# Kernel optimization log

Hardware: AMD Instinct MI355X
Metric: run time of the kernel (lower is better)

The kernel has to match this reference:

```python
import jax, jax.numpy as jnp
import numpy as np

LN_EPS = 1e-5

def _layer_norm(x, gamma, beta):
    m = jnp.mean(x, axis=-1, keepdims=True)
    v = jnp.mean((x - m) ** 2, axis=-1, keepdims=True)
    return (x - m) / jnp.sqrt(v + LN_EPS) * gamma + beta

def setup_inputs() -> dict:
    key = jax.random.key(0)
    k1, k2, k3 = jax.random.split(key, 3)
    N, E, D = 8192, 4096, 128
    node_embeddings = jax.random.normal(k1, (N, D), dtype=jnp.float32)
    target_matrix = jax.random.normal(k2, (N, N), dtype=jnp.float32)
    hypergraph_matrix = jax.random.randint(k3, (N, E), 0, 2, dtype=jnp.int32)
    ln_gamma = jnp.ones((D,), dtype=jnp.float32)
    ln_beta = jnp.zeros((D,), dtype=jnp.float32)
    return {
        "node_embeddings": node_embeddings,
        "target_matrix": target_matrix,
        "ln_gamma": ln_gamma,
        "ln_beta": ln_beta,
        "hypergraph_matrix": hypergraph_matrix,
        "num_layers": 3,
    }

def reference(node_embeddings, target_matrix, ln_gamma, ln_beta, hypergraph_matrix, num_layers):
    x = node_embeddings  # [N, D]
    for _ in range(num_layers):
        t = jnp.matmul(target_matrix, x)        # [N, D]
        x = jnp.matmul(target_matrix.T, t)      # [N, D]
        x = _layer_norm(x, ln_gamma, ln_beta)
        # dropout is identity in eval mode
    # per-hyperedge masked mean over nodes, vectorized as a dense GEMV-style reduce
    h = (hypergraph_matrix > 0).astype(x.dtype)            # [N, E]
    counts = jnp.sum(h, axis=0)                            # [E]
    sums = jnp.einsum('ne,nd->ed', h, x)                   # [E, D]
    means = sums / counts[:, None]                         # [E, D]
    return jnp.max(means, axis=0)                          # [D]
```

## Files before the change

### kernel.cpp

```cpp
#include <hip/hip_runtime.h>
#include <cstdint>
#include <cstddef>

typedef __attribute__((ext_vector_type(8))) short short8;
typedef __attribute__((ext_vector_type(4))) short short4v;
typedef __attribute__((ext_vector_type(4))) float float4v;
typedef __attribute__((ext_vector_type(4))) int int4v;
typedef unsigned short ushort_t;

__device__ __forceinline__ ushort_t f2bf(float f) {
  unsigned u = __builtin_bit_cast(unsigned, f);
  u = (u + 0x7FFFu + ((u >> 16) & 1u)) >> 16;
  return (ushort_t)u;
}
__device__ __forceinline__ float bf2f(ushort_t h) {
  unsigned u = ((unsigned)h) << 16;
  return __builtin_bit_cast(float, u);
}

__device__ __forceinline__ void gld_lds16(const void* g, void* l) {
  __builtin_amdgcn_global_load_lds(
      (const __attribute__((address_space(1))) void*)g,
      (__attribute__((address_space(3))) void*)l, 16, 0, 0);
}

__global__ __launch_bounds__(256, 3) void gemm_tn(
    const ushort_t* __restrict__ A, const ushort_t* __restrict__ B,
    float* __restrict__ P, int M, int N, int K) {
  __shared__ ushort_t As[128 * 64];
  __shared__ ushort_t Bs[128 * 64];
  const int tid = threadIdx.x;
  const int lane = tid & 63;
  const int wave = tid >> 6;
  const int wm = (wave & 1) * 64;
  const int wn = (wave >> 1) * 64;
  const int m0 = blockIdx.x * 128;
  const int n0 = blockIdx.y * 128;
  int t0, tl;
  if (blockIdx.z < 8) { t0 = blockIdx.z * 11; tl = 11; }
  else { t0 = 88 + (blockIdx.z - 8) * 10; tl = 10; }
  float* __restrict__ Pc = P + (size_t)blockIdx.z * M * N;

  float4v acc[4][4] = {};

  for (int t = t0; t < t0 + tl; t++) {
    const ushort_t* Ag = A + (size_t)m0 * K + t * 64;
    const ushort_t* Bg = B + (size_t)n0 * K + t * 64;
#pragma unroll
    for (int i = 0; i < 4; i++) {
      int f = i * 4096 + tid * 16;
      int r = f >> 7;
      int cb = f & 127;
      gld_lds16((const char*)(Ag + (size_t)r * K) + cb, (char*)As + f);
      gld_lds16((const char*)(Bg + (size_t)r * K) + cb, (char*)Bs + f);
    }
    __syncthreads();
#pragma unroll
    for (int ks = 0; ks < 64; ks += 32) {
      short8 af[4], bfr[4];
      const int kr = ks + (lane >> 4) * 8;
      const int l15 = lane & 15;
#pragma unroll
      for (int im = 0; im < 4; im++)
        af[im] = *(const short8*)&As[(wm + im * 16 + l15) * 64 + kr];
#pragma unroll
      for (int in = 0; in < 4; in++)
        bfr[in] = *(const short8*)&Bs[(wn + in * 16 + l15) * 64 + kr];
#pragma unroll
      for (int im = 0; im < 4; im++)
#pragma unroll
        for (int in = 0; in < 4; in++)
          acc[im][in] = __builtin_amdgcn_mfma_f32_16x16x32_bf16(
              af[im], bfr[in], acc[im][in], 0, 0, 0);
    }
    __syncthreads();
  }
  const int cn = lane & 15;
  const int cr = (lane >> 4) * 4;
#pragma unroll
  for (int im = 0; im < 4; im++)
#pragma unroll
    for (int in = 0; in < 4; in++)
#pragma unroll
      for (int r = 0; r < 4; r++) {
        int m = wm + im * 16 + cr + r;
        int n = wn + in * 16 + cn;
        Pc[(size_t)(m0 + m) * N + (n0 + n)] = acc[im][in][r];
      }
}

__global__ __launch_bounds__(256, 3) void gemm_nn(
    const ushort_t* __restrict__ A, const ushort_t* __restrict__ B,
    float* __restrict__ P, int M, int N, int K) {
  __shared__ ushort_t As[128 * 64];
  __shared__ ushort_t Bs[64 * 128];
  const int tid = threadIdx.x;
  const int lane = tid & 63;
  const int wave = tid >> 6;
  const int wm = (wave & 1) * 64;
  const int wn = (wave >> 1) * 64;
  const int m0 = blockIdx.x * 128;
  const int n0 = blockIdx.y * 128;
  int t0, tl;
  if (blockIdx.z < 8) { t0 = blockIdx.z * 11; tl = 11; }
  else { t0 = 88 + (blockIdx.z - 8) * 10; tl = 10; }
  float* __restrict__ Pc = P + (size_t)blockIdx.z * M * N;

  int brow[4], bcol[4];
#pragma unroll
  for (int i = 0; i < 4; i++) {
    const int c = i * 256 + tid;
    brow[i] = ((c >> 6) << 2) | ((c >> 1) & 3);
    bcol[i] = (((c >> 3) & 7) << 4) | ((c & 1) << 3);
  }
  const int l15 = lane & 15;
  const int hi = lane >> 4;
  const unsigned BsB =
      (unsigned)(uintptr_t)(__attribute__((address_space(3))) void*)Bs;
  const unsigned trb = BsB + (unsigned)(hi * 2048) + (unsigned)(l15 * 8);

  float4v acc[4][4] = {};

  for (int t = t0; t < t0 + tl; t++) {
    const ushort_t* Ag = A + (size_t)m0 * K + t * 64;
    const ushort_t* Bg = B + (size_t)(t * 64) * N + n0;
#pragma unroll
    for (int i = 0; i < 4; i++) {
      int f = i * 4096 + tid * 16;
      int r = f >> 7;
      int cb = f & 127;
      gld_lds16((const char*)(Ag + (size_t)r * K) + cb, (char*)As + f);
      gld_lds16((const char*)(Bg + (size_t)brow[i] * N + bcol[i]),
                (char*)Bs + f);
    }
    __syncthreads();
#pragma unroll
    for (int ks = 0; ks < 64; ks += 32) {
      short8 af[4];
      const int kr = ks + hi * 8;
#pragma unroll
      for (int im = 0; im < 4; im++)
        af[im] = *(const short8*)&As[(wm + im * 16 + l15) * 64 + kr];
      short4v r0[4], r1[4];
      const unsigned tb = trb + (unsigned)((ks >> 2) * 1024) + (unsigned)(wn * 8);
#pragma unroll
      for (int in = 0; in < 4; in++) {
        asm volatile(
            "ds_read_b64_tr_b16 %0, %2\n\t"
            "ds_read_b64_tr_b16 %1, %2 offset:1024"
            : "=&v"(r0[in]), "=&v"(r1[in])
            : "v"(tb + (unsigned)(in * 128)));
      }
      asm volatile("s_waitcnt lgkmcnt(0)" ::: "memory");
      __builtin_amdgcn_sched_barrier(0);
#pragma unroll
      for (int im = 0; im < 4; im++)
#pragma unroll
        for (int in = 0; in < 4; in++) {
          short8 bf8 = __builtin_shufflevector(r0[in], r1[in],
                                               0, 1, 2, 3, 4, 5, 6, 7);
          acc[im][in] = __builtin_amdgcn_mfma_f32_16x16x32_bf16(
              af[im], bf8, acc[im][in], 0, 0, 0);
        }
    }
    __syncthreads();
  }
  const int cn = lane & 15;
  const int cr = (lane >> 4) * 4;
#pragma unroll
  for (int im = 0; im < 4; im++)
#pragma unroll
    for (int in = 0; in < 4; in++)
#pragma unroll
      for (int r = 0; r < 4; r++) {
        int m = wm + im * 16 + cr + r;
        int n = wn + in * 16 + cn;
        Pc[(size_t)(m0 + m) * N + (n0 + n)] = acc[im][in][r];
      }
}

__global__ __launch_bounds__(256) void cast32_k(
    const float* __restrict__ src, ushort_t* __restrict__ dst) {
  const size_t i = ((size_t)blockIdx.x * 256 + threadIdx.x) * 8;
  float4v a = *(const float4v*)(src + i);
  float4v b = *(const float4v*)(src + i + 4);
  ushort_t o[8];
  o[0] = f2bf(a.x); o[1] = f2bf(a.y); o[2] = f2bf(a.z); o[3] = f2bf(a.w);
  o[4] = f2bf(b.x); o[5] = f2bf(b.y); o[6] = f2bf(b.z); o[7] = f2bf(b.w);
  *(short8*)&dst[i] = *(const short8*)o;
}

__global__ __launch_bounds__(256) void dualcast_f32_k(
    const float* __restrict__ src, ushort_t* __restrict__ dstN,
    ushort_t* __restrict__ dstT, int R, int C) {
  __shared__ float tile[64][65];
  const int c0 = blockIdx.x * 64, r0 = blockIdx.y * 64;
  const int tr = threadIdx.x >> 2, cs = (threadIdx.x & 3) * 16;
  const float* s = src + (size_t)(r0 + tr) * C + c0 + cs;
  float v[16];
#pragma unroll
  for (int j = 0; j < 16; j += 4) {
    float4v t4 = *(const float4v*)(s + j);
    v[j] = t4.x; v[j + 1] = t4.y; v[j + 2] = t4.z; v[j + 3] = t4.w;
  }
  if (dstN) {
    ushort_t o[16];
#pragma unroll
    for (int j = 0; j < 16; j++) o[j] = f2bf(v[j]);
    ushort_t* d = dstN + (size_t)(r0 + tr) * C + c0 + cs;
    *(short8*)d = *(const short8*)&o[0];
    *(short8*)(d + 8) = *(const short8*)&o[8];
  }
#pragma unroll
  for (int j = 0; j < 16; j++) tile[tr][cs + j] = v[j];
  __syncthreads();
  const int tc = threadIdx.x >> 2, rs = (threadIdx.x & 3) * 16;
  ushort_t o[16];
#pragma unroll
  for (int j = 0; j < 16; j++) o[j] = f2bf(tile[rs + j][tc]);
  ushort_t* d = dstT + (size_t)(c0 + tc) * R + r0 + rs;
  *(short8*)d = *(const short8*)&o[0];
  *(short8*)(d + 8) = *(const short8*)&o[8];
}

__global__ __launch_bounds__(256) void tcast_i32_k(
    const int* __restrict__ src, ushort_t* __restrict__ dstT,
    float* __restrict__ partial, int R, int C) {
  __shared__ float tile[64][65];
  const int c0 = blockIdx.x * 64, r0 = blockIdx.y * 64;
  const int tr = threadIdx.x >> 2, cs = (threadIdx.x & 3) * 16;
  const int* s = src + (size_t)(r0 + tr) * C + c0 + cs;
#pragma unroll
  for (int j = 0; j < 16; j += 4) {
    int4v t4 = *(const int4v*)(s + j);
    tile[tr][cs + j] = t4.x > 0 ? 1.f : 0.f;
    tile[tr][cs + j + 1] = t4.y > 0 ? 1.f : 0.f;
    tile[tr][cs + j + 2] = t4.z > 0 ? 1.f : 0.f;
    tile[tr][cs + j + 3] = t4.w > 0 ? 1.f : 0.f;
  }
  __syncthreads();
  const int tc = threadIdx.x >> 2, rs = (threadIdx.x & 3) * 16;
  ushort_t o[16];
#pragma unroll
  for (int j = 0; j < 16; j++) o[j] = f2bf(tile[rs + j][tc]);
  ushort_t* d = dstT + (size_t)(c0 + tc) * R + r0 + rs;
  *(short8*)d = *(const short8*)&o[0];
  *(short8*)(d + 8) = *(const short8*)&o[8];
  if (threadIdx.x < 64) {
    float sum = 0.f;
#pragma unroll
    for (int r = 0; r < 64; r++) sum += tile[r][threadIdx.x];
    partial[(size_t)(r0 >> 6) * C + c0 + threadIdx.x] = sum;
  }
}

__global__ __launch_bounds__(256) void counts2_k(
    const float* __restrict__ partial, float* __restrict__ counts, int E) {
  const int e = blockIdx.x * 256 + threadIdx.x;
  float s = 0.f;
  for (int r = 0; r < 128; r++) s += partial[(size_t)r * E + e];
  counts[e] = s;
}

__global__ __launch_bounds__(256) void cast_k(
    const float* __restrict__ P, ushort_t* __restrict__ out, int MN) {
  const int i = (blockIdx.x * 256 + threadIdx.x) * 8;
  float4v a = {0.f, 0.f, 0.f, 0.f}, b = {0.f, 0.f, 0.f, 0.f};
  for (int sp = 0; sp < 12; sp++) {
    a += *(const float4v*)&P[(size_t)sp * MN + i];
    b += *(const float4v*)&P[(size_t)sp * MN + i + 4];
  }
  ushort_t o[8];
  o[0] = f2bf(a.x); o[1] = f2bf(a.y); o[2] = f2bf(a.z); o[3] = f2bf(a.w);
  o[4] = f2bf(b.x); o[5] = f2bf(b.y); o[6] = f2bf(b.z); o[7] = f2bf(b.w);
  *(short8*)&out[i] = *(const short8*)o;
}

__global__ __launch_bounds__(256) void ln_cast_k(
    const float* __restrict__ P, const float* __restrict__ gamma,
    const float* __restrict__ beta, ushort_t* __restrict__ xT, int Ncols) {
  __shared__ float ssum[8][32], ssq[8][32];
  const int c = threadIdx.x & 31;
  const int q = threadIdx.x >> 5;
  const int m = blockIdx.x * 32 + c;
  const size_t DN = (size_t)128 * Ncols;
  float vloc[16];
  float s = 0.f, sq = 0.f;
#pragma unroll
  for (int j = 0; j < 16; j++) {
    const int d = q * 16 + j;
    float v = 0.f;
    for (int sp = 0; sp < 12; sp++)
      v += P[(size_t)sp * DN + (size_t)d * Ncols + m];
    vloc[j] = v; s += v; sq += v * v;
  }
  ssum[q][c] = s;
  ssq[q][c] = sq;
  __syncthreads();
  float S = 0.f, SQ = 0.f;
#pragma unroll
  for (int r = 0; r < 8; r++) { S += ssum[r][c]; SQ += ssq[r][c]; }
  const float mean = S * (1.f / 128.f);
  const float var = SQ * (1.f / 128.f) - mean * mean;
  const float inv = rsqrtf(var + 1e-5f);
#pragma unroll
  for (int j = 0; j < 16; j++) {
    const int d = q * 16 + j;
    xT[(size_t)d * Ncols + m] = f2bf((vloc[j] - mean) * inv * gamma[d] + beta[d]);
  }
}

__global__ __launch_bounds__(256) void mm1_k(
    const float* __restrict__ P, const float* __restrict__ counts,
    float* __restrict__ pm, int EMN) {
  __shared__ float4v red[8][32];
  const int el = threadIdx.x >> 5;
  const int l32 = threadIdx.x & 31;
  const int e0 = blockIdx.x * 16;
  float4v vmax = {-3.4e38f, -3.4e38f, -3.4e38f, -3.4e38f};
  for (int ee = el; ee < 16; ee += 8) {
    const int e = e0 + ee;
    float4v s = {0.f, 0.f, 0.f, 0.f};
    for (int sp = 0; sp < 12; sp++)
      s += *(const float4v*)&P[(size_t)sp * EMN + (size_t)e * 128 + l32 * 4];
    const float inv = 1.f / counts[e];
    s *= inv;
    vmax.x = fmaxf(vmax.x, s.x); vmax.y = fmaxf(vmax.y, s.y);
    vmax.z = fmaxf(vmax.z, s.z); vmax.w = fmaxf(vmax.w, s.w);
  }
  red[el][l32] = vmax;
  __syncthreads();
  if (el == 0) {
    float4v m = red[0][l32];
#pragma unroll
    for (int r = 1; r < 8; r++) {
      float4v t = red[r][l32];
      m.x = fmaxf(m.x, t.x); m.y = fmaxf(m.y, t.y);
      m.z = fmaxf(m.z, t.z); m.w = fmaxf(m.w, t.w);
    }
    *(float4v*)&pm[(size_t)blockIdx.x * 128 + l32 * 4] = m;
  }
}

__global__ __launch_bounds__(128) void mm2_k(
    const float* __restrict__ pm, float* __restrict__ out, int B) {
  const int d = threadIdx.x;
  float v = -3.4e38f;
  for (int b = 0; b < B; b++) v = fmaxf(v, pm[b * 128 + d]);
  out[d] = v;
}

extern "C" void kernel_launch(void* const* d_in, const int* in_sizes, int n_in,
                              void* d_out, int out_size, void* d_ws,
                              size_t ws_size, hipStream_t stream) {
  const float* x0 = (const float*)d_in[0];
  const float* T = (const float*)d_in[1];
  const float* gamma = (const float*)d_in[2];
  const float* beta = (const float*)d_in[3];
  const int* h = (const int*)d_in[4];
  float* out = (float*)d_out;

  const int N = 8192, E = 4096, D = 128, K = 8192, S = 12;

  char* ws = (char*)d_ws;
  size_t off = 0;
  auto alloc = [&](size_t bytes) {
    char* p = ws + off;
    off += (bytes + 255) & ~(size_t)255;
    return p;
  };
  ushort_t* Tb = (ushort_t*)alloc((size_t)N * N * 2);
  ushort_t* hT = (ushort_t*)alloc((size_t)E * N * 2);
  ushort_t* xT = (ushort_t*)alloc((size_t)D * N * 2);
  ushort_t* tT = (ushort_t*)alloc((size_t)D * N * 2);
  float* P = (float*)alloc((size_t)S * D * N * 4);
  float* counts = (float*)alloc((size_t)E * 4);
  float* partial = (float*)alloc((size_t)(N / 64) * E * 4);
  float* pm = (float*)alloc((size_t)256 * D * 4);
  (void)ws_size;

  cast32_k<<<(int)((size_t)N * N / 2048), 256, 0, stream>>>(T, Tb);
  dualcast_f32_k<<<dim3(D / 64, N / 64), 256, 0, stream>>>(x0, nullptr, xT, N, D);
  tcast_i32_k<<<dim3(E / 64, N / 64), 256, 0, stream>>>(h, hT, partial, N, E);
  counts2_k<<<E / 256, 256, 0, stream>>>(partial, counts, E);

  for (int layer = 0; layer < 3; layer++) {
    gemm_tn<<<dim3(1, N / 128, S), 256, 0, stream>>>(xT, Tb, P, D, N, K);
    cast_k<<<D * N / (256 * 8), 256, 0, stream>>>(P, tT, D * N);
    gemm_nn<<<dim3(1, N / 128, S), 256, 0, stream>>>(tT, Tb, P, D, N, K);
    ln_cast_k<<<N / 32, 256, 0, stream>>>(P, gamma, beta, xT, N);
  }
  gemm_tn<<<dim3(E / 128, 1, S), 256, 0, stream>>>(hT, xT, P, E, D, K);
  mm1_k<<<E / 16, 256, 0, stream>>>(P, counts, pm, E * D);
  mm2_k<<<1, 128, 0, stream>>>(pm, out, E / 16);
}
```

Baseline: 829.0 us.

## Store bf16 target matrix and hyperedge mask in 64x64 tiled layout for contiguous GEMM loads

```diff
diff --git a/kernel.cpp b/kernel.cpp
--- a/kernel.cpp
+++ b/kernel.cpp
@@ -24,9 +24,10 @@
       (__attribute__((address_space(3))) void*)l, 16, 0, 0);
 }
 
+
 __global__ __launch_bounds__(256, 3) void gemm_tn(
     const ushort_t* __restrict__ A, const ushort_t* __restrict__ B,
-    float* __restrict__ P, int M, int N, int K) {
+    float* __restrict__ P, int M, int N, int K, int ATILED, int BTILED) {
   __shared__ ushort_t As[128 * 64];
   __shared__ ushort_t Bs[128 * 64];
   const int tid = threadIdx.x;
@@ -41,18 +42,38 @@
   else { t0 = 88 + (blockIdx.z - 8) * 10; tl = 10; }
   float* __restrict__ Pc = P + (size_t)blockIdx.z * M * N;
 
+  const char* aP[4];
+  const char* bP[4];
+  size_t aStep, bStep;
+#pragma unroll
+  for (int i = 0; i < 4; i++) {
+    const int f = i * 4096 + tid * 16;
+    if (ATILED) {
+      aP[i] = (const char*)A +
+              (((size_t)((m0 >> 6) + (f >> 13)) * (size_t)(K >> 6)) << 13) +
+              (f & 8191);
+    } else {
+      aP[i] = (const char*)A + ((size_t)(m0 + (f >> 7)) * K) * 2 + (f & 127);
+    }
+    if (BTILED) {
+      bP[i] = (const char*)B +
+              (((size_t)((n0 >> 6) + (f >> 13)) * (size_t)(K >> 6)) << 13) +
+              (f & 8191);
+    } else {
+      bP[i] = (const char*)B + ((size_t)(n0 + (f >> 7)) * K) * 2 + (f & 127);
+    }
+  }
+  aStep = ATILED ? 8192 : 128;
+  bStep = BTILED ? 8192 : 128;
+
   float4v acc[4][4] = {};
 
   for (int t = t0; t < t0 + tl; t++) {
-    const ushort_t* Ag = A + (size_t)m0 * K + t * 64;
-    const ushort_t* Bg = B + (size_t)n0 * K + t * 64;
 #pragma unroll
     for (int i = 0; i < 4; i++) {
-      int f = i * 4096 + tid * 16;
-      int r = f >> 7;
-      int cb = f & 127;
-      gld_lds16((const char*)(Ag + (size_t)r * K) + cb, (char*)As + f);
-      gld_lds16((const char*)(Bg + (size_t)r * K) + cb, (char*)Bs + f);
+      const int f = i * 4096 + tid * 16;
+      gld_lds16(aP[i] + (size_t)t * aStep, (char*)As + f);
+      gld_lds16(bP[i] + (size_t)t * bStep, (char*)Bs + f);
     }
     __syncthreads();
 #pragma unroll
@@ -106,13 +127,20 @@
   else { t0 = 88 + (blockIdx.z - 8) * 10; tl = 10; }
   float* __restrict__ Pc = P + (size_t)blockIdx.z * M * N;
 
-  int brow[4], bcol[4];
+  const char* aP[4];
+  const char* bP[4];
 #pragma unroll
   for (int i = 0; i < 4; i++) {
     const int c = i * 256 + tid;
-    brow[i] = ((c >> 6) << 2) | ((c >> 1) & 3);
-    bcol[i] = (((c >> 3) & 7) << 4) | ((c & 1) << 3);
-  }
+    const int f = i * 4096 + tid * 16;
+    const int brow = ((c >> 6) << 2) | ((c >> 1) & 3);
+    const int bcol = (((c >> 3) & 7) << 4) | ((c & 1) << 3);
+    const int bsrc = (bcol & 64 ? 8192 : 0) + brow * 128 + (bcol & 63) * 2;
+    bP[i] = (const char*)B + ((size_t)(n0 >> 6) << 13) + bsrc;
+    aP[i] = (const char*)A + ((size_t)(m0 + (f >> 7)) * K) * 2 + (f & 127);
+  }
+  const size_t bStep = (size_t)(N >> 6) << 13;
+
   const int l15 = lane & 15;
   const int hi = lane >> 4;
   const unsigned BsB =
@@ -122,16 +150,11 @@
   float4v acc[4][4] = {};
 
   for (int t = t0; t < t0 + tl; t++) {
-    const ushort_t* Ag = A + (size_t)m0 * K + t * 64;
-    const ushort_t* Bg = B + (size_t)(t * 64) * N + n0;
 #pragma unroll
     for (int i = 0; i < 4; i++) {
-      int f = i * 4096 + tid * 16;
-      int r = f >> 7;
-      int cb = f & 127;
-      gld_lds16((const char*)(Ag + (size_t)r * K) + cb, (char*)As + f);
-      gld_lds16((const char*)(Bg + (size_t)brow[i] * N + bcol[i]),
-                (char*)Bs + f);
+      const int f = i * 4096 + tid * 16;
+      gld_lds16(aP[i] + (size_t)t * 128, (char*)As + f);
+      gld_lds16(bP[i] + (size_t)t * bStep, (char*)Bs + f);
     }
     __syncthreads();
 #pragma unroll
@@ -179,15 +202,29 @@
       }
 }
 
-__global__ __launch_bounds__(256) void cast32_k(
+__global__ __launch_bounds__(256) void repack_T_k(
     const float* __restrict__ src, ushort_t* __restrict__ dst) {
-  const size_t i = ((size_t)blockIdx.x * 256 + threadIdx.x) * 8;
-  float4v a = *(const float4v*)(src + i);
-  float4v b = *(const float4v*)(src + i + 4);
-  ushort_t o[8];
-  o[0] = f2bf(a.x); o[1] = f2bf(a.y); o[2] = f2bf(a.z); o[3] = f2bf(a.w);
-  o[4] = f2bf(b.x); o[5] = f2bf(b.y); o[6] = f2bf(b.z); o[7] = f2bf(b.w);
-  *(short8*)&dst[i] = *(const short8*)o;
+  __shared__ ushort_t tile[32][520];
+  const int bx = blockIdx.x;
+  const int by = blockIdx.y;
+  const int t = threadIdx.x;
+  const int r = t >> 3, cs = (t & 7) * 64;
+  const float* s = src + (size_t)(by * 32 + r) * 8192 + bx * 512 + cs;
+#pragma unroll
+  for (int j = 0; j < 64; j += 4) {
+    float4v v = *(const float4v*)(s + j);
+    short4v o;
+    o.x = (short)f2bf(v.x); o.y = (short)f2bf(v.y);
+    o.z = (short)f2bf(v.z); o.w = (short)f2bf(v.w);
+    *(short4v*)&tile[r][cs + j] = o;
+  }
+  __syncthreads();
+  const int q = t & 7;
+  ushort_t* d = dst + ((size_t)(by >> 1) * 128 + bx * 8) * 4096 +
+                (size_t)(by & 1) * 2048 + r * 64 + q * 8;
+#pragma unroll
+  for (int jj = 0; jj < 8; jj++)
+    *(short8*)(d + (size_t)jj * 4096) = *(const short8*)&tile[r][jj * 64 + q * 8];
 }
 
 __global__ __launch_bounds__(256) void dualcast_f32_k(
@@ -243,7 +280,8 @@
   ushort_t o[16];
 #pragma unroll
   for (int j = 0; j < 16; j++) o[j] = f2bf(tile[rs + j][tc]);
-  ushort_t* d = dstT + (size_t)(c0 + tc) * R + r0 + rs;
+  ushort_t* d = dstT + (((size_t)(c0 >> 6) * (size_t)(R >> 6) + (r0 >> 6)) << 12) +
+                tc * 64 + rs;
   *(short8*)d = *(const short8*)&o[0];
   *(short8*)(d + 8) = *(const short8*)&o[8];
   if (threadIdx.x < 64) {
@@ -379,18 +417,18 @@
   float* pm = (float*)alloc((size_t)256 * D * 4);
   (void)ws_size;
 
-  cast32_k<<<(int)((size_t)N * N / 2048), 256, 0, stream>>>(T, Tb);
+  repack_T_k<<<dim3(16, 256), 256, 0, stream>>>(T, Tb);
   dualcast_f32_k<<<dim3(D / 64, N / 64), 256, 0, stream>>>(x0, nullptr, xT, N, D);
   tcast_i32_k<<<dim3(E / 64, N / 64), 256, 0, stream>>>(h, hT, partial, N, E);
   counts2_k<<<E / 256, 256, 0, stream>>>(partial, counts, E);
 
   for (int layer = 0; layer < 3; layer++) {
-    gemm_tn<<<dim3(1, N / 128, S), 256, 0, stream>>>(xT, Tb, P, D, N, K);
+    gemm_tn<<<dim3(1, N / 128, S), 256, 0, stream>>>(xT, Tb, P, D, N, K, 0, 1);
     cast_k<<<D * N / (256 * 8), 256, 0, stream>>>(P, tT, D * N);
     gemm_nn<<<dim3(1, N / 128, S), 256, 0, stream>>>(tT, Tb, P, D, N, K);
     ln_cast_k<<<N / 32, 256, 0, stream>>>(P, gamma, beta, xT, N);
   }
-  gemm_tn<<<dim3(E / 128, 1, S), 256, 0, stream>>>(hT, xT, P, E, D, K);
+  gemm_tn<<<dim3(E / 128, 1, S), 256, 0, stream>>>(hT, xT, P, E, D, K, 1, 0);
   mm1_k<<<E / 16, 256, 0, stream>>>(P, counts, pm, E * D);
   mm2_k<<<1, 128, 0, stream>>>(pm, out, E / 16);
 }
```

Result: no change. 824.3 us (-0.6%).
